# Kernel optimization log

Measured on AMD Instinct MI355X. Metric: run time of the kernel, lower is better.

Reference implementation:

```python
import jax, jax.numpy as jnp
import numpy as np

DIM = 768
NUM_HEADS = 12
HEAD_DIM = DIM // NUM_HEADS
SCALE = HEAD_DIM ** -0.5
B, N = 16, 640  # N = 8*8 + 24*24


def setup_inputs() -> dict:
    key = jax.random.key(0)
    ks = jax.random.split(key, 4)
    x = jax.random.normal(ks[0], (B, N, DIM), dtype=jnp.float32)
    # weights stored input-major: y = x @ W + b (equiv. to torch Linear with W = weight.T)
    qkv_w = jax.random.normal(ks[1], (DIM, 3 * DIM), dtype=jnp.float32) * (DIM ** -0.5)
    qkv_b = jnp.zeros((3 * DIM,), dtype=jnp.float32)
    proj_w = jax.random.normal(ks[2], (DIM, DIM), dtype=jnp.float32) * (DIM ** -0.5)
    proj_b = jnp.zeros((DIM,), dtype=jnp.float32)
    w = jnp.ones((2,), dtype=jnp.float32)
    return {"x": x, "qkv_w": qkv_w, "qkv_b": qkv_b, "proj_w": proj_w,
            "proj_b": proj_b, "w": w, "t_h": 8, "t_w": 8, "s_h": 24, "s_w": 24}


def reference(x, qkv_w, qkv_b, proj_w, proj_b, w, t_h, t_w, s_h, s_w):
    b, n, c = x.shape
    qkv = (x @ qkv_w + qkv_b).reshape(b, n, 3, NUM_HEADS, HEAD_DIM)
    qkv = jnp.transpose(qkv, (2, 0, 3, 1, 4))  # [3, B, H, N, D]
    q, k, v = qkv[0], qkv[1], qkv[2]
    attn = jnp.einsum('bhnd,bhmd->bhnm', q, k) * SCALE  # [B,H,N,N]
    attn0 = jax.nn.softmax(attn, axis=-1)
    attn1 = jnp.square(jax.nn.relu(attn))
    ws = jax.nn.softmax(w)  # exp(w_i)/sum(exp(w)) blend weights
    attn = attn0 * ws[0] + attn1 * ws[1]
    out = jnp.einsum('bhnm,bhmd->bhnd', attn, v)  # [B,H,N,D]
    out = jnp.transpose(out, (0, 2, 1, 3)).reshape(b, n, c)
    return out @ proj_w + proj_b
```

## Files before the change

### kernel.cpp

```cpp
#include <hip/hip_runtime.h>
#include <hip/hip_bf16.h>

typedef __attribute__((ext_vector_type(8))) short short8;
typedef __attribute__((ext_vector_type(4))) float floatx4;
typedef __hip_bfloat16 bf16;

#define DIM 768
#define NH 12
#define HD 64
#define BB 16
#define NN 640
#define BH (BB*NH)
#define MROWS (BB*NN)
#define QKVN (3*DIM)
#define QSCALE 0.18033688011113205f
#define LN2SQ 0.4804530139182014f

#define CVT_BLK (MROWS*DIM/4/256)
#define TRQ_BLK ((QKVN/32)*(DIM/32))
#define TRP_BLK ((DIM/32)*(DIM/32))

__device__ __forceinline__ floatx4 mfma16(short8 a, short8 b, floatx4 c) {
    return __builtin_amdgcn_mfma_f32_16x16x32_bf16(a, b, c, 0, 0, 0);
}

__device__ __forceinline__ void async_ld16(const bf16* g, bf16* l) {
    __builtin_amdgcn_global_load_lds(
        (const __attribute__((address_space(1))) void*)g,
        (__attribute__((address_space(3))) void*)l, 16, 0, 0);
}

__device__ __forceinline__ unsigned pack_trunc(float a, float b) {
    return __builtin_amdgcn_perm(__float_as_uint(b), __float_as_uint(a), 0x07060302u);
}

__device__ __forceinline__ unsigned pack_rne(float a, float b) {
    unsigned sa = (unsigned)__bfloat16_as_ushort(__float2bfloat16(a));
    unsigned sb = (unsigned)__bfloat16_as_ushort(__float2bfloat16(b));
    return sa | (sb << 16);
}

__device__ __forceinline__ float fexp2(float x) {
#if __has_builtin(__builtin_amdgcn_exp2f)
    return __builtin_amdgcn_exp2f(x);
#else
    return exp2f(x);
#endif
}

__global__ void prep_all(const float* __restrict__ x,
                         const float* __restrict__ qkv_w,
                         const float* __restrict__ proj_w,
                         bf16* __restrict__ xb,
                         bf16* __restrict__ qwT,
                         bf16* __restrict__ pwT)
{
    __shared__ float tile[32][33];
    const int id = blockIdx.x;
    const int t = threadIdx.x;

    if (id < CVT_BLK) {
        int i = id * 256 + t;
        float4 v = ((const float4*)x)[i];
        *(uint2*)(xb + (size_t)i * 4) =
            make_uint2(pack_rne(v.x, v.y), pack_rne(v.z, v.w));
        return;
    }

    const float* src; bf16* dst; int C, bx, by;
    if (id < CVT_BLK + TRQ_BLK) {
        int j = id - CVT_BLK;
        bx = j % (QKVN/32); by = j / (QKVN/32);
        src = qkv_w; dst = qwT; C = QKVN;
    } else {
        int j = id - CVT_BLK - TRQ_BLK;
        bx = j % (DIM/32); by = j / (DIM/32);
        src = proj_w; dst = pwT; C = DIM;
    }
    const int R = DIM;
    const int tx = t & 31, ty = t >> 5;
    for (int j = 0; j < 4; ++j)
        tile[ty + j*8][tx] = src[(size_t)(by*32 + ty + j*8) * C + bx*32 + tx];
    __syncthreads();
    for (int j = 0; j < 4; ++j)
        dst[(size_t)(bx*32 + ty + j*8) * R + by*32 + tx] = __float2bfloat16(tile[tx][ty + j*8]);
}

__global__ __launch_bounds__(512, 2) void gemm_qkv(
    const bf16* __restrict__ A, const bf16* __restrict__ B, const float* __restrict__ bias,
    bf16* __restrict__ outb, bf16* __restrict__ vTo)
{
    constexpr int K = DIM;
    constexpr int N = QKVN;
    constexpr int GX = N / 192;
    constexpr int NWG = GX * (MROWS / 256);
    constexpr int CHUNK = NWG / 8;

    __shared__ __align__(16) bf16 As[2][256*64];
    __shared__ __align__(16) bf16 Bs[2][192*64];

    const int t = threadIdx.x;
    const int lane = t & 63, wave = t >> 6;
    const int l15 = lane & 15, quad = lane >> 4;
    const int wm = wave >> 1;
    const int wn = wave & 1;

    int lin = blockIdx.x;
    lin = (lin & 7) * CHUNK + (lin >> 3);
    const int m0 = (lin / GX) * 256, n0 = (lin % GX) * 192;

    floatx4 acc[4][6];
    floatx4 zero = {0.f, 0.f, 0.f, 0.f};
#pragma unroll
    for (int i = 0; i < 4; ++i)
#pragma unroll
        for (int j = 0; j < 6; ++j)
            acc[i][j] = zero;

    const int trow = t >> 3;
    const int gc = ((t & 7) ^ (trow & 7)) << 3;
    const bf16* Ag = A + (size_t)(m0 + trow) * K + gc;
    const bf16* Bg = B + (size_t)(n0 + trow) * K + gc;
    const int tb = t * 8;

#define STG_A(buf,s,tcol) async_ld16(Ag + (size_t)(s)*64*K + (tcol), &As[buf][(s)*4096 + tb])
#define STG_B(buf,s,tcol) async_ld16(Bg + (size_t)(s)*64*K + (tcol), &Bs[buf][(s)*4096 + tb])

    const int sw8 = (quad ^ (l15 & 7)) << 3;
    const int aoff = (wm*64 + l15) * 64 + sw8;
    const int boff = (wn*96 + l15) * 64 + sw8;

    short8 afr[4][2], bfr[2][2];

#define RD_A(buf) do { \
    _Pragma("unroll") \
    for (int f = 0; f < 4; ++f) { \
        afr[f][0] = *(const short8*)&As[buf][aoff + f*1024]; \
        afr[f][1] = *(const short8*)&As[buf][(aoff + f*1024) ^ 32]; \
    } } while (0)

#define RD_B2(buf, fp) do { \
    bfr[0][0] = *(const short8*)&Bs[buf][boff + (2*(fp))*1024]; \
    bfr[0][1] = *(const short8*)&Bs[buf][(boff + (2*(fp))*1024) ^ 32]; \
    bfr[1][0] = *(const short8*)&Bs[buf][boff + (2*(fp)+1)*1024]; \
    bfr[1][1] = *(const short8*)&Bs[buf][(boff + (2*(fp)+1)*1024) ^ 32]; \
    } while (0)

#define MFMA16(fp) do { \
    __builtin_amdgcn_s_setprio(1); \
    _Pragma("unroll") \
    for (int fm = 0; fm < 4; ++fm) { \
        acc[fm][2*(fp)]   = mfma16(bfr[0][0], afr[fm][0], acc[fm][2*(fp)]); \
        acc[fm][2*(fp)+1] = mfma16(bfr[1][0], afr[fm][0], acc[fm][2*(fp)+1]); \
    } \
    _Pragma("unroll") \
    for (int fm = 0; fm < 4; ++fm) { \
        acc[fm][2*(fp)]   = mfma16(bfr[0][1], afr[fm][1], acc[fm][2*(fp)]); \
        acc[fm][2*(fp)+1] = mfma16(bfr[1][1], afr[fm][1], acc[fm][2*(fp)+1]); \
    } \
    __builtin_amdgcn_s_setprio(0); \
} while (0)

#define BAR_LG0() do { \
    __builtin_amdgcn_s_barrier(); \
    asm volatile("s_waitcnt lgkmcnt(0)" ::: "memory"); \
    __builtin_amdgcn_sched_barrier(0); \
} while (0)

    STG_A(0,0,0); STG_A(0,1,0); STG_A(0,2,0); STG_A(0,3,0);
    STG_B(0,0,0); STG_B(0,1,0); STG_B(0,2,0);
    STG_A(1,0,64); STG_A(1,1,64); STG_A(1,2,64); STG_A(1,3,64);
    asm volatile("s_waitcnt vmcnt(4)" ::: "memory");
    __builtin_amdgcn_s_barrier();

    for (int it = 0; it < 6; ++it) {
        const int kb = it * 128;
        const bool more = (it < 5);
        RD_A(0); RD_B2(0, 0);
        STG_B(1,0,kb+64); STG_B(1,1,kb+64); STG_B(1,2,kb+64);
        asm volatile("s_waitcnt lgkmcnt(8)" ::: "memory");
        BAR_LG0();
        MFMA16(0);
        __builtin_amdgcn_sched_barrier(0);
        __builtin_amdgcn_s_barrier();
        RD_B2(0, 1);
        if (more) { STG_A(0,0,kb+128); STG_A(0,1,kb+128); STG_A(0,2,kb+128); STG_A(0,3,kb+128); }
        BAR_LG0();
        MFMA16(1);
        __builtin_amdgcn_sched_barrier(0);
        __builtin_amdgcn_s_barrier();
        RD_B2(0, 2);
        BAR_LG0();
        MFMA16(2);
        __builtin_amdgcn_sched_barrier(0);
        if (more) { asm volatile("s_waitcnt vmcnt(4)" ::: "memory"); }
        else      { asm volatile("s_waitcnt vmcnt(0)" ::: "memory"); }
        __builtin_amdgcn_s_barrier();
        RD_A(1); RD_B2(1, 0);
        if (more) { STG_B(0,0,kb+128); STG_B(0,1,kb+128); STG_B(0,2,kb+128); }
        asm volatile("s_waitcnt lgkmcnt(8)" ::: "memory");
        BAR_LG0();
        MFMA16(0);
        __builtin_amdgcn_sched_barrier(0);
        __builtin_amdgcn_s_barrier();
        RD_B2(1, 1);
        if (more) { STG_A(1,0,kb+192); STG_A(1,1,kb+192); STG_A(1,2,kb+192); STG_A(1,3,kb+192); }
        BAR_LG0();
        MFMA16(1);
        __builtin_amdgcn_sched_barrier(0);
        __builtin_amdgcn_s_barrier();
        RD_B2(1, 2);
        BAR_LG0();
        MFMA16(2);
        __builtin_amdgcn_sched_barrier(0);
        if (more) { asm volatile("s_waitcnt vmcnt(4)" ::: "memory"); }
        __builtin_amdgcn_s_barrier();
    }
#undef RD_A
#undef RD_B2
#undef MFMA16
#undef BAR_LG0
#undef STG_A
#undef STG_B

    const int mb = m0 + wm * 64;
    const int nb = n0 + wn * 96;

    if (n0 >= 2*DIM) {
        bf16* S = &As[0][0] + wave * 2048;
        unsigned short* Su = (unsigned short*)S;
        const int batch = mb / NN;
        const int tokb = mb % NN;
        const int dl = lane >> 2, cc = (lane & 3) * 16;
#pragma unroll
        for (int fn = 0; fn < 6; ++fn) {
            int cb = nb + fn*16;
            int bh = batch * NH + ((cb - 2*DIM) >> 6);
            int dbase = cb & 63;
            float4 bv = *(const float4*)(bias + cb + quad*4);
            float bvr[4] = {bv.x, bv.y, bv.z, bv.w};
#pragma unroll
            for (int fm = 0; fm < 4; ++fm) {
#pragma unroll
                for (int r = 0; r < 4; ++r) {
                    float v = acc[fm][fn][r] + bvr[r];
                    Su[(quad*4 + r)*72 + fm*16 + l15] =
                        (unsigned short)(__float_as_uint(v) >> 16);
                }
            }
            uint4 r0 = *(const uint4*)(S + dl*72 + cc);
            uint4 r1 = *(const uint4*)(S + dl*72 + cc + 8);
            bf16* dst = vTo + ((size_t)bh * HD + dbase + dl) * NN + tokb + cc;
            *(uint4*)dst = r0;
            *(uint4*)(dst + 8) = r1;
        }
        return;
    }

#pragma unroll
    for (int fm = 0; fm < 4; ++fm) {
        int m = mb + fm*16 + l15;
        bf16* row = outb + (size_t)m * N;
#pragma unroll
        for (int fn = 0; fn < 6; ++fn) {
            int n = nb + fn*16 + quad*4;
            float4 bv = *(const float4*)(bias + n);
            float v0 = acc[fm][fn][0] + bv.x;
            float v1 = acc[fm][fn][1] + bv.y;
            float v2 = acc[fm][fn][2] + bv.z;
            float v3 = acc[fm][fn][3] + bv.w;
            if (n < DIM) { v0 *= QSCALE; v1 *= QSCALE; v2 *= QSCALE; v3 *= QSCALE; }
            *(uint2*)(row + n) = make_uint2(pack_rne(v0, v1), pack_rne(v2, v3));
        }
    }
}

template<int MODE>
__global__ __launch_bounds__(256) void gemm_bt(
    const bf16* __restrict__ A, const bf16* __restrict__ B, const float* __restrict__ bias,
    int M, int N, int K,
    bf16* __restrict__ outb, bf16* __restrict__ vTo, float* __restrict__ outf)
{
    __shared__ __align__(16) bf16 As[2][128*64];
    __shared__ __align__(16) bf16 Bs[2][128*64];

    const int t = threadIdx.x;
    const int lane = t & 63, wave = t >> 6;
    const int l15 = lane & 15, quad = lane >> 4;
    const int wm = (wave >> 1) * 64, wn = (wave & 1) * 64;

    constexpr int GX  = (MODE == 0) ? (QKVN/128) : (DIM/128);
    constexpr int NWG = GX * (MROWS/128);
    constexpr int CHUNK = NWG / 8;
    int lin = blockIdx.y * GX + blockIdx.x;
    lin = (lin & 7) * CHUNK + (lin >> 3);
    const int m0 = (lin / GX) * 128, n0 = (lin % GX) * 128;

    floatx4 acc[4][4];
    floatx4 zero = {0.f, 0.f, 0.f, 0.f};
    for (int i = 0; i < 4; ++i)
        for (int j = 0; j < 4; ++j)
            acc[i][j] = zero;

    const int trow = t >> 3;
    const int gc = ((t & 7) ^ (trow & 7)) << 3;
    const bf16* aA = A + (size_t)(m0 + trow) * K + gc;
    const bf16* aB = B + (size_t)(n0 + trow) * K + gc;
    const int lb = wave * 512;

    for (int s = 0; s < 4; ++s) {
        async_ld16(aA + (size_t)s*32*K, &As[0][s*2048 + lb]);
        async_ld16(aB + (size_t)s*32*K, &Bs[0][s*2048 + lb]);
    }

    const int sw = l15 & 7;
    const int nit = K >> 6;
    for (int kt = 0; kt < nit; ++kt) {
        const int cur = kt & 1;
        __syncthreads();
        if (kt + 1 < nit) {
            const bf16* pA = aA + (size_t)(kt+1)*64;
            const bf16* pB = aB + (size_t)(kt+1)*64;
            for (int s = 0; s < 4; ++s) {
                async_ld16(pA + (size_t)s*32*K, &As[cur^1][s*2048 + lb]);
                async_ld16(pB + (size_t)s*32*K, &Bs[cur^1][s*2048 + lb]);
            }
        }
        short8 af0[4], af1[4], bf0[4], bf1[4];
        for (int fm = 0; fm < 4; ++fm) {
            int base = (wm + fm*16 + l15) * 64 + ((quad ^ sw) << 3);
            af0[fm] = *(const short8*)(&As[cur][base]);
            af1[fm] = *(const short8*)(&As[cur][base ^ 32]);
        }
        for (int fn = 0; fn < 4; ++fn) {
            int base = (wn + fn*16 + l15) * 64 + ((quad ^ sw) << 3);
            bf0[fn] = *(const short8*)(&Bs[cur][base]);
            bf1[fn] = *(const short8*)(&Bs[cur][base ^ 32]);
        }
        for (int fm = 0; fm < 4; ++fm)
            for (int fn = 0; fn < 4; ++fn) {
                acc[fm][fn] = mfma16(bf0[fn], af0[fm], acc[fm][fn]);
                acc[fm][fn] = mfma16(bf1[fn], af1[fm], acc[fm][fn]);
            }
    }

    for (int fm = 0; fm < 4; ++fm) {
        int m = m0 + wm + fm*16 + l15;
        float* row = outf + (size_t)m * N;
        for (int fn = 0; fn < 4; ++fn) {
            int n = n0 + wn + fn*16 + quad*4;
            float4 bv = *(const float4*)(bias + n);
            float4 v;
            v.x = acc[fm][fn][0] + bv.x;
            v.y = acc[fm][fn][1] + bv.y;
            v.z = acc[fm][fn][2] + bv.z;
            v.w = acc[fm][fn][3] + bv.w;
            *(float4*)(row + n) = v;
        }
    }
}

__global__ __launch_bounds__(256) void attn_kernel(
    const bf16* __restrict__ qkv, const bf16* __restrict__ vT,
    const float* __restrict__ w2, bf16* __restrict__ ao)
{
    int lin = blockIdx.y * BH + blockIdx.x;
    int j = lin >> 3;
    const int bh = (lin & 7) + 8 * (j / 10);
    const int qt = j % 10;
    const int b = bh / NH, h = bh - b * NH;
    const int t = threadIdx.x;
    const int wave = t >> 6, lane = t & 63;
    const int l15 = lane & 15, quad = lane >> 4;
    const int qrow0 = qt * 64 + wave * 16;

    float w0 = w2[0], w1 = w2[1];
    float wmx = fmaxf(w0, w1);
    float e0 = __expf(w0 - wmx), e1 = __expf(w1 - wmx);
    float ws0 = e0 / (e0 + e1);
    float ws1 = (1.0f - ws0) * LN2SQ;

    __shared__ __align__(16) bf16 Kb[2][64*64];
    __shared__ __align__(16) bf16 Vb[2][64*64];
    __shared__ __align__(16) bf16 Ps[4][16*72];
    __shared__ __align__(16) bf16 Pr[4][16*72];

    const bf16* kb = qkv + (size_t)(b*NN)*QKVN + DIM + h*HD;
    const bf16* vb = vT + (size_t)bh * HD * NN;

    const bf16* qr = qkv + (size_t)(b*NN + qrow0 + l15) * QKVN + h*HD;
    short8 aq0 = *(const short8*)(qr + quad*8);
    short8 aq1 = *(const short8*)(qr + 32 + quad*8);

    const int srow = t >> 3;
    const int gc   = ((lane & 7) ^ (lane >> 3)) << 3;
    const bf16* kst = kb + (size_t)srow * QKVN + gc;
    const bf16* vst = vb + (size_t)srow * NN + gc;
    const int lb0 = (wave * 64) * 8;
    const int lb1 = (256 + wave * 64) * 8;

    async_ld16(kst,                     &Kb[0][lb0]);
    async_ld16(kst + (size_t)32 * QKVN, &Kb[0][lb1]);
    async_ld16(vst,                     &Vb[0][lb0]);
    async_ld16(vst + (size_t)32 * NN,   &Vb[0][lb1]);

    floatx4 zero = {0.f, 0.f, 0.f, 0.f};
    floatx4 accS[4], accR[4];
    for (int i = 0; i < 4; ++i) { accS[i] = zero; accR[i] = zero; }
    float lsum = 0.f;

    const int sw = l15 & 7;
    const int fbase = l15 * 64 + ((quad ^ sw) << 3);

    unsigned* PsW = (unsigned*)&Ps[wave][0];
    unsigned* PrW = (unsigned*)&Pr[wave][0];
    const int wb = l15*36 + quad*2;
    const bf16* PsR = &Ps[wave][l15*72 + quad*8];
    const bf16* PrR = &Pr[wave][l15*72 + quad*8];

#pragma unroll 2
    for (int kt = 0; kt < 10; ++kt) {
        const int cur = kt & 1;
        __syncthreads();
        if (kt + 1 < 10) {
            kst += (size_t)64 * QKVN;
            vst += 64;
            async_ld16(kst,                     &Kb[cur^1][lb0]);
            async_ld16(kst + (size_t)32 * QKVN, &Kb[cur^1][lb1]);
            async_ld16(vst,                     &Vb[cur^1][lb0]);
            async_ld16(vst + (size_t)32 * NN,   &Vb[cur^1][lb1]);
        }

        const bf16* Kc = &Kb[cur][0];
        const bf16* Vc = &Vb[cur][0];

        floatx4 s[4];
        for (int I = 0; I < 4; ++I) {
            short8 aklo = *(const short8*)(Kc + fbase + I*1024);
            short8 akhi = *(const short8*)(Kc + ((fbase + I*1024) ^ 32));
            s[I] = zero;
            s[I] = mfma16(aklo, aq0, s[I]);
            s[I] = mfma16(akhi, aq1, s[I]);
        }

        short8 bvlo[4], bvhi[4];
        for (int dt = 0; dt < 4; ++dt) {
            bvlo[dt] = *(const short8*)(Vc + fbase + dt*1024);
            bvhi[dt] = *(const short8*)(Vc + ((fbase + dt*1024) ^ 32));
        }

        for (int I = 0; I < 4; ++I) {
            float ex[4], rq[4];
            for (int r = 0; r < 4; ++r) {
                ex[r] = fexp2(s[I][r]);
                float m = fmaxf(s[I][r], 0.f);
                rq[r] = m * m;
                lsum += ex[r];
            }
            *(uint2*)(PsW + wb + I*8) = make_uint2(pack_trunc(ex[0],ex[1]), pack_trunc(ex[2],ex[3]));
            *(uint2*)(PrW + wb + I*8) = make_uint2(pack_trunc(rq[0],rq[1]), pack_trunc(rq[2],rq[3]));
        }

        short8 paSlo = *(const short8*)PsR;
        short8 paShi = *(const short8*)(PsR + 32);
        short8 paRlo = *(const short8*)PrR;
        short8 paRhi = *(const short8*)(PrR + 32);

        for (int dt = 0; dt < 4; ++dt) {
            accS[dt] = mfma16(paSlo, bvlo[dt], accS[dt]);
            accS[dt] = mfma16(paShi, bvhi[dt], accS[dt]);
            accR[dt] = mfma16(paRlo, bvlo[dt], accR[dt]);
            accR[dt] = mfma16(paRhi, bvhi[dt], accR[dt]);
        }
    }

    lsum += __shfl_xor(lsum, 16);
    lsum += __shfl_xor(lsum, 32);
    float invq[4];
    for (int r = 0; r < 4; ++r)
        invq[r] = 1.0f / __shfl(lsum, quad*4 + r);

    for (int dt = 0; dt < 4; ++dt) {
        for (int r = 0; r < 4; ++r) {
            float v = ws0 * accS[dt][r] * invq[r] + ws1 * accR[dt][r];
            int tok = qrow0 + quad*4 + r;
            ao[((size_t)(b * NN + tok)) * DIM + h * HD + dt*16 + l15] = __float2bfloat16(v);
        }
    }
}


extern "C" void kernel_launch(void* const* d_in, const int* in_sizes, int n_in,
                              void* d_out, int out_size, void* d_ws, size_t ws_size,
                              hipStream_t stream) {
    const float* x      = (const float*)d_in[0];
    const float* qkv_w  = (const float*)d_in[1];
    const float* qkv_b  = (const float*)d_in[2];
    const float* proj_w = (const float*)d_in[3];
    const float* proj_b = (const float*)d_in[4];
    const float* w2     = (const float*)d_in[5];
    float* out = (float*)d_out;

    bf16* xb   = (bf16*)d_ws;
    bf16* qwT  = xb   + (size_t)MROWS * DIM;
    bf16* pwT  = qwT  + (size_t)QKVN * DIM;
    bf16* qkvb = pwT  + (size_t)DIM * DIM;
    bf16* vT   = qkvb + (size_t)MROWS * QKVN;
    bf16* ao   = xb;

    prep_all<<<CVT_BLK + TRQ_BLK + TRP_BLK, 256, 0, stream>>>(
        x, qkv_w, proj_w, xb, qwT, pwT);

    gemm_qkv<<<dim3((QKVN/192) * (MROWS/256)), 512, 0, stream>>>(
        xb, qwT, qkv_b, qkvb, vT);

    attn_kernel<<<dim3(BH, NN / 64), 256, 0, stream>>>(qkvb, vT, w2, ao);

    gemm_bt<1><<<dim3(DIM / 128, MROWS / 128), 256, 0, stream>>>(
        ao, pwT, proj_b, MROWS, DIM, DIM, nullptr, nullptr, out);
}
```

Before: 216.6 us.

## Interleave QK MFMA with softmax in attention loop and raise MFMA priority

Restructures the attention inner loop so the QK MFMAs for two key sub-tiles are issued, then their exp/relu² work and LDS writes run while the next two sub-tiles' MFMAs proceed. The PV MFMAs are split into lo/hi halves with the V loads interleaved between them, and s_setprio raises wave priority around MFMA bursts to encourage overlap across waves. It also changes the P staging row pitch from 72 to 68 bf16 to alter LDS bank mapping. The aim is to overlap VALU transcendental work with matrix-core work, at the cost of more sensitivity to compiler scheduling and possible new bank conflicts from the changed pitch.

```diff
diff --git a/kernel.cpp b/kernel.cpp
--- a/kernel.cpp
+++ b/kernel.cpp
@@ -382,8 +382,8 @@
 
     __shared__ __align__(16) bf16 Kb[2][64*64];
     __shared__ __align__(16) bf16 Vb[2][64*64];
-    __shared__ __align__(16) bf16 Ps[4][16*72];
-    __shared__ __align__(16) bf16 Pr[4][16*72];
+    __shared__ __align__(16) bf16 Ps[4][16*68];
+    __shared__ __align__(16) bf16 Pr[4][16*68];
 
     const bf16* kb = qkv + (size_t)(b*NN)*QKVN + DIM + h*HD;
     const bf16* vb = vT + (size_t)bh * HD * NN;
@@ -414,9 +414,26 @@
 
     unsigned* PsW = (unsigned*)&Ps[wave][0];
     unsigned* PrW = (unsigned*)&Pr[wave][0];
-    const int wb = l15*36 + quad*2;
-    const bf16* PsR = &Ps[wave][l15*72 + quad*8];
-    const bf16* PrR = &Pr[wave][l15*72 + quad*8];
+    const int wb = l15*34 + quad*2;
+    const bf16* PsR = &Ps[wave][l15*68 + quad*8];
+    const bf16* PrR = &Pr[wave][l15*68 + quad*8];
+
+#define QK1(sv, I) do { \
+    short8 aklo = *(const short8*)(Kc + fbase + (I)*1024); \
+    short8 akhi = *(const short8*)(Kc + ((fbase + (I)*1024) ^ 32)); \
+    sv = mfma16(aklo, aq0, sv); \
+    sv = mfma16(akhi, aq1, sv); \
+} while (0)
+
+#define SMWR(I, sv) do { \
+    float ex0 = fexp2(sv[0]), ex1 = fexp2(sv[1]); \
+    float ex2 = fexp2(sv[2]), ex3 = fexp2(sv[3]); \
+    float m0_ = fmaxf(sv[0], 0.f), m1_ = fmaxf(sv[1], 0.f); \
+    float m2_ = fmaxf(sv[2], 0.f), m3_ = fmaxf(sv[3], 0.f); \
+    lsum += (ex0 + ex1) + (ex2 + ex3); \
+    *(uint2*)(PsW + wb + (I)*8) = make_uint2(pack_trunc(ex0,ex1), pack_trunc(ex2,ex3)); \
+    *(uint2*)(PrW + wb + (I)*8) = make_uint2(pack_trunc(m0_*m0_,m1_*m1_), pack_trunc(m2_*m2_,m3_*m3_)); \
+} while (0)
 
 #pragma unroll 2
     for (int kt = 0; kt < 10; ++kt) {
@@ -434,45 +451,47 @@
         const bf16* Kc = &Kb[cur][0];
         const bf16* Vc = &Vb[cur][0];
 
-        floatx4 s[4];
-        for (int I = 0; I < 4; ++I) {
-            short8 aklo = *(const short8*)(Kc + fbase + I*1024);
-            short8 akhi = *(const short8*)(Kc + ((fbase + I*1024) ^ 32));
-            s[I] = zero;
-            s[I] = mfma16(aklo, aq0, s[I]);
-            s[I] = mfma16(akhi, aq1, s[I]);
-        }
-
-        short8 bvlo[4], bvhi[4];
-        for (int dt = 0; dt < 4; ++dt) {
+        floatx4 s0 = zero, s1 = zero;
+        __builtin_amdgcn_s_setprio(1);
+        QK1(s0, 0); QK1(s1, 1);
+        __builtin_amdgcn_s_setprio(0);
+        SMWR(0, s0); SMWR(1, s1);
+        floatx4 s2 = zero, s3 = zero;
+        __builtin_amdgcn_s_setprio(1);
+        QK1(s2, 2); QK1(s3, 3);
+        __builtin_amdgcn_s_setprio(0);
+        short8 bvlo[4];
+#pragma unroll
+        for (int dt = 0; dt < 4; ++dt)
             bvlo[dt] = *(const short8*)(Vc + fbase + dt*1024);
+        short8 paSlo = *(const short8*)PsR;
+        short8 paRlo = *(const short8*)PrR;
+        SMWR(2, s2); SMWR(3, s3);
+        __builtin_amdgcn_s_setprio(1);
+#pragma unroll
+        for (int dt = 0; dt < 4; ++dt)
+            accS[dt] = mfma16(paSlo, bvlo[dt], accS[dt]);
+#pragma unroll
+        for (int dt = 0; dt < 4; ++dt)
+            accR[dt] = mfma16(paRlo, bvlo[dt], accR[dt]);
+        __builtin_amdgcn_s_setprio(0);
+        short8 bvhi[4];
+#pragma unroll
+        for (int dt = 0; dt < 4; ++dt)
             bvhi[dt] = *(const short8*)(Vc + ((fbase + dt*1024) ^ 32));
-        }
-
-        for (int I = 0; I < 4; ++I) {
-            float ex[4], rq[4];
-            for (int r = 0; r < 4; ++r) {
-                ex[r] = fexp2(s[I][r]);
-                float m = fmaxf(s[I][r], 0.f);
-                rq[r] = m * m;
-                lsum += ex[r];
-            }
-            *(uint2*)(PsW + wb + I*8) = make_uint2(pack_trunc(ex[0],ex[1]), pack_trunc(ex[2],ex[3]));
-            *(uint2*)(PrW + wb + I*8) = make_uint2(pack_trunc(rq[0],rq[1]), pack_trunc(rq[2],rq[3]));
-        }
-
-        short8 paSlo = *(const short8*)PsR;
         short8 paShi = *(const short8*)(PsR + 32);
-        short8 paRlo = *(const short8*)PrR;
         short8 paRhi = *(const short8*)(PrR + 32);
-
-        for (int dt = 0; dt < 4; ++dt) {
-            accS[dt] = mfma16(paSlo, bvlo[dt], accS[dt]);
+        __builtin_amdgcn_s_setprio(1);
+#pragma unroll
+        for (int dt = 0; dt < 4; ++dt)
             accS[dt] = mfma16(paShi, bvhi[dt], accS[dt]);
-            accR[dt] = mfma16(paRlo, bvlo[dt], accR[dt]);
+#pragma unroll
+        for (int dt = 0; dt < 4; ++dt)
             accR[dt] = mfma16(paRhi, bvhi[dt], accR[dt]);
-        }
-    }
+        __builtin_amdgcn_s_setprio(0);
+    }
+#undef QK1
+#undef SMWR
 
     lsum += __shfl_xor(lsum, 16);
     lsum += __shfl_xor(lsum, 32);
```

Result: slower. 233.3 us (+7.7%).
